# Kernel optimization log

Measured on AMD Instinct MI355X. Metric: run time of the kernel, lower is better.

The kernel has to match this reference:

```python
import jax, jax.numpy as jnp
import numpy as np
from jax import lax

DIM = 384
NH = 8
HD = DIM // NH
M = 16          # num_anchors
B = 16
HH = 64
WW = 64
N = HH * WW
STD = 0.02


def setup_inputs() -> dict:
    key = jax.random.key(0)
    ks = jax.random.split(key, 12)
    rn = lambda k, shape: (jax.random.normal(k, shape, jnp.float32) * STD)
    return {
        "x": jax.random.normal(ks[0], (B, N, DIM), jnp.float32),
        "H": HH,
        "W": WW,
        "saliency_w": rn(ks[1], (DIM, 1)),
        "saliency_b": jnp.zeros((1,), jnp.float32),
        "anchor_seeds": rn(ks[2], (1, M, DIM)),
        "w_q_agg": rn(ks[3], (DIM, DIM)),
        "w_kv_agg": rn(ks[4], (DIM, 2 * DIM)),
        "w_q_self": rn(ks[5], (DIM, DIM)),
        "w_kv_self": rn(ks[6], (DIM, 2 * DIM)),
        "w_q_bcast": rn(ks[7], (DIM, DIM)),
        "w_kv_bcast": rn(ks[8], (DIM, 2 * DIM)),
        "dw_kernel": rn(ks[9], (DIM, 1, 3, 3)),  # depthwise conv, OIHW with I=1
        "w_proj": rn(ks[10], (DIM, DIM)),
    }


def _mhsa(q_in, kv_in, wq, wkv):
    """Multi-head cross attention. q_in: [B,Lq,C], kv_in: [B,Lk,C]."""
    b, lq, c = q_in.shape
    lk = kv_in.shape[1]
    scale = HD ** -0.5
    q = (q_in @ wq).reshape(b, lq, NH, HD)
    kv = (kv_in @ wkv).reshape(b, lk, 2, NH, HD)
    k, v = kv[:, :, 0], kv[:, :, 1]
    attn = jnp.einsum("bqhd,bkhd->bhqk", q, k) * scale
    attn = jax.nn.softmax(attn, axis=-1)
    out = jnp.einsum("bhqk,bkhd->bqhd", attn, v).reshape(b, lq, c)
    return out


def reference(x, H, W, saliency_w, saliency_b, anchor_seeds,
              w_q_agg, w_kv_agg, w_q_self, w_kv_self,
              w_q_bcast, w_kv_bcast, dw_kernel, w_proj):
    b, n, c = x.shape
    # saliency gating
    sal = jax.nn.sigmoid(x @ saliency_w + saliency_b)  # [B,N,1]
    x_sal = x * sal
    # stage 1: anchors aggregate from saliency-gated tokens
    anchors = jnp.broadcast_to(anchor_seeds, (b, M, c))
    anchors = anchors + _mhsa(anchors, x_sal, w_q_agg, w_kv_agg)
    # stage 2: anchor self-attention
    anchors = anchors + _mhsa(anchors, anchors, w_q_self, w_kv_self)
    # stage 3: broadcast anchors back to all tokens
    global_out = _mhsa(x, anchors, w_q_bcast, w_kv_bcast)
    # depthwise 3x3 conv on the 2D token map
    x2d = x.reshape(b, H, W, c).transpose(0, 3, 1, 2)  # NCHW
    local = lax.conv_general_dilated(
        x2d, dw_kernel, window_strides=(1, 1), padding="SAME",
        feature_group_count=c,
        dimension_numbers=("NCHW", "OIHW", "NCHW"))
    local = local.transpose(0, 2, 3, 1).reshape(b, n, c)
    return (global_out + local) @ w_proj
```

## Files before the change

kernel.cpp:

```cpp
#include <hip/hip_runtime.h>
#include <hip/hip_bf16.h>

#define SCALE 0.14433756729740643f

typedef __attribute__((ext_vector_type(8))) short bf16x8;
typedef __attribute__((ext_vector_type(4))) float f32x4;

template <typename T> __device__ inline T cvt_from_f(float v);
template <> __device__ inline float cvt_from_f<float>(float v) { return v; }
template <> __device__ inline __hip_bfloat16 cvt_from_f<__hip_bfloat16>(float v) { return __float2bfloat16(v); }

__device__ inline void gload16(const void* g, void* l) {
  __builtin_amdgcn_global_load_lds((const __attribute__((address_space(1))) void*)g,
                                   (__attribute__((address_space(3))) void*)l, 16, 0, 0);
}

__device__ inline int xcd_flat(int nwg) {
  int flat = (blockIdx.z * gridDim.y + blockIdx.y) * gridDim.x + blockIdx.x;
  int per = nwg >> 3;
  return (flat & 7) * per + (flat >> 3);
}

__global__ __launch_bounds__(256) void prep(const float* __restrict__ x,
                                            const float* __restrict__ wsal,
                                            const float* __restrict__ bsal,
                                            __hip_bfloat16* __restrict__ xb,
                                            float* __restrict__ sal) {
  int wave = threadIdx.x >> 6, lane = threadIdx.x & 63;
  size_t row = (size_t)blockIdx.x * 4 + wave;
  const float* xr = x + row * 384;
  float xs[6];
  float part = 0.f;
#pragma unroll
  for (int j = 0; j < 6; j++) {
    int c = lane + 64 * j;
    xs[j] = xr[c];
    part += xs[j] * wsal[c];
  }
#pragma unroll
  for (int off = 32; off >= 1; off >>= 1) part += __shfl_xor(part, off);
  float s = 1.f / (1.f + __expf(-(part + bsal[0])));
#pragma unroll
  for (int j = 0; j < 6; j++) {
    int c = lane + 64 * j;
    xb[row * 384 + c] = __float2bfloat16(xs[j]);
  }
  if (lane == 0) sal[row] = s;
}

__global__ void wcast_tv(const float* __restrict__ w, __hip_bfloat16* __restrict__ wt) {
  int idx = blockIdx.x * 256 + threadIdx.x;
  if (idx >= 384 * 384) return;
  int n = idx / 384, k = idx % 384;
  wt[idx] = __float2bfloat16(w[(size_t)k * 768 + 384 + n]);
}

template <int K, typename OT, int BSHIFT>
__global__ __launch_bounds__(256) void gemm_mfma(const __hip_bfloat16* __restrict__ A,
                                                 const __hip_bfloat16* __restrict__ BT,
                                                 OT* __restrict__ out, int Ncols,
                                                 size_t btBatchStride) {
  __shared__ __align__(16) __hip_bfloat16 Asl[128][32];
  __shared__ __align__(16) __hip_bfloat16 Bsl[128][32];
  int nf = xcd_flat(gridDim.x * gridDim.y);
  int bX = nf % gridDim.x, bY = nf / gridDim.x;
  int tid = threadIdx.x;
  int lane = tid & 63;
  int w = tid >> 6;
  int wr = w >> 1, wc = w & 1;
  int fr = lane & 15, fq = lane >> 4;
  int rowBase = bY * 128, colBase = bX * 128;
  const __hip_bfloat16* BTb = BT + (size_t)(rowBase >> BSHIFT) * btBatchStride;

  int r1 = tid >> 2, kc1 = tid & 3;
  int r2 = (tid + 256) >> 2;

  char* aB1 = (char*)Asl + (size_t)(w * 64) * 16;
  char* aB2 = (char*)Asl + (size_t)(256 + w * 64) * 16;
  char* bB1 = (char*)Bsl + (size_t)(w * 64) * 16;
  char* bB2 = (char*)Bsl + (size_t)(256 + w * 64) * 16;

  const __hip_bfloat16* a1 = A + (size_t)(rowBase + r1) * K + kc1 * 8;
  const __hip_bfloat16* a2 = A + (size_t)(rowBase + r2) * K + kc1 * 8;
  const __hip_bfloat16* b1 = BTb + (size_t)(colBase + r1) * K + kc1 * 8;
  const __hip_bfloat16* b2 = BTb + (size_t)(colBase + r2) * K + kc1 * 8;

  f32x4 acc[4][4] = {};

  for (int kk = 0; kk < K; kk += 32) {
    gload16(a1 + kk, aB1);
    gload16(a2 + kk, aB2);
    gload16(b1 + kk, bB1);
    gload16(b2 + kk, bB2);
    __syncthreads();
    bf16x8 af[4], bfv[4];
#pragma unroll
    for (int m = 0; m < 4; m++) af[m] = *(const bf16x8*)&Asl[wr * 64 + m * 16 + fr][fq * 8];
#pragma unroll
    for (int n = 0; n < 4; n++) bfv[n] = *(const bf16x8*)&Bsl[wc * 64 + n * 16 + fr][fq * 8];
#pragma unroll
    for (int m = 0; m < 4; m++)
#pragma unroll
      for (int n = 0; n < 4; n++)
        acc[m][n] = __builtin_amdgcn_mfma_f32_16x16x32_bf16(af[m], bfv[n], acc[m][n], 0, 0, 0);
    __syncthreads();
  }

#pragma unroll
  for (int m = 0; m < 4; m++) {
    int row0 = rowBase + wr * 64 + m * 16 + fq * 4;
#pragma unroll
    for (int n = 0; n < 4; n++) {
      int col = colBase + wc * 64 + n * 16 + fr;
      f32x4 v = acc[m][n];
#pragma unroll
      for (int r = 0; r < 4; r++) out[(size_t)(row0 + r) * Ncols + col] = cvt_from_f<OT>(v[r]);
    }
  }
}

__global__ __launch_bounds__(256) void gemm_vlog(const __hip_bfloat16* __restrict__ A,
                                                 const __hip_bfloat16* __restrict__ BT,
                                                 __hip_bfloat16* __restrict__ vT,
                                                 __hip_bfloat16* __restrict__ lgT,
                                                 const float* __restrict__ rowScale) {
  constexpr int K = 384;
  __shared__ __align__(16) __hip_bfloat16 Asl[128][32];
  __shared__ __align__(16) __hip_bfloat16 Bsl[128][32];
  int nf = xcd_flat(2048);
  int bX = nf & 3, bY = nf >> 2;
  int tid = threadIdx.x;
  int lane = tid & 63;
  int w = tid >> 6;
  int wr = w >> 1, wc = w & 1;
  int fr = lane & 15, fq = lane >> 4;
  int rowBase = bY * 128, colBase = bX * 128;

  int r1 = tid >> 2, kc1 = tid & 3;
  int r2 = (tid + 256) >> 2;

  char* aB1 = (char*)Asl + (size_t)(w * 64) * 16;
  char* aB2 = (char*)Asl + (size_t)(256 + w * 64) * 16;
  char* bB1 = (char*)Bsl + (size_t)(w * 64) * 16;
  char* bB2 = (char*)Bsl + (size_t)(256 + w * 64) * 16;

  const __hip_bfloat16* a1 = A + (size_t)(rowBase + r1) * K + kc1 * 8;
  const __hip_bfloat16* a2 = A + (size_t)(rowBase + r2) * K + kc1 * 8;
  const __hip_bfloat16* b1 = BT + (size_t)(colBase + r1) * K + kc1 * 8;
  const __hip_bfloat16* b2 = BT + (size_t)(colBase + r2) * K + kc1 * 8;

  f32x4 acc[4][4] = {};

  for (int kk = 0; kk < K; kk += 32) {
    gload16(a1 + kk, aB1);
    gload16(a2 + kk, aB2);
    gload16(b1 + kk, bB1);
    gload16(b2 + kk, bB2);
    __syncthreads();
    bf16x8 af[4], bfv[4];
#pragma unroll
    for (int m = 0; m < 4; m++) af[m] = *(const bf16x8*)&Asl[wr * 64 + m * 16 + fr][fq * 8];
#pragma unroll
    for (int n = 0; n < 4; n++) bfv[n] = *(const bf16x8*)&Bsl[wc * 64 + n * 16 + fr][fq * 8];
#pragma unroll
    for (int m = 0; m < 4; m++)
#pragma unroll
      for (int n = 0; n < 4; n++)
        acc[m][n] = __builtin_amdgcn_mfma_f32_16x16x32_bf16(af[m], bfv[n], acc[m][n], 0, 0, 0);
    __syncthreads();
  }

  float sv[4][4];
#pragma unroll
  for (int m = 0; m < 4; m++)
#pragma unroll
    for (int r = 0; r < 4; r++)
      sv[m][r] = rowScale[rowBase + wr * 64 + m * 16 + fq * 4 + r];

  if (bX < 3) {
#pragma unroll
    for (int m = 0; m < 4; m++) {
      int row0 = rowBase + wr * 64 + m * 16 + fq * 4;
      int bb = row0 >> 12;
      int n0 = row0 & 4095;
#pragma unroll
      for (int n = 0; n < 4; n++) {
        int col = colBase + wc * 64 + n * 16 + fr;
        __hip_bfloat16 tb[4];
#pragma unroll
        for (int r = 0; r < 4; r++) tb[r] = __float2bfloat16(acc[m][n][r] * sv[m][r]);
        *(unsigned long long*)(vT + ((size_t)bb * 384 + col) * 4096 + n0) = *(unsigned long long*)tb;
      }
    }
  } else {
#pragma unroll
    for (int m = 0; m < 4; m++) {
      int row0 = rowBase + wr * 64 + m * 16 + fq * 4;
      int bb = row0 >> 12;
      int n0 = row0 & 4095;
#pragma unroll
      for (int n = 0; n < 4; n++) {
        int col = wc * 64 + n * 16 + fr;
        __hip_bfloat16 tb[4];
#pragma unroll
        for (int r = 0; r < 4; r++) tb[r] = __float2bfloat16(acc[m][n][r] * sv[m][r]);
        *(unsigned long long*)(lgT + ((size_t)bb * 128 + col) * 4096 + n0) = *(unsigned long long*)tb;
      }
    }
  }
}

__global__ __launch_bounds__(256) void gemm_pv(const __hip_bfloat16* __restrict__ PT,
                                               const __hip_bfloat16* __restrict__ vT,
                                               float* __restrict__ pbuf) {
  __shared__ __align__(16) __hip_bfloat16 Asl[128][32];
  __shared__ __align__(16) __hip_bfloat16 Bsl[128][32];
  int nf = xcd_flat(384);
  int bX = nf % 3, bY = (nf / 3) & 15, kz = nf / 48;
  int tid = threadIdx.x;
  int lane = tid & 63;
  int w = tid >> 6;
  int wr = w >> 1, wc = w & 1;
  int fr = lane & 15, fq = lane >> 4;
  int rowBase = bY * 128, colBase = bX * 128;
  const __hip_bfloat16* BTb = vT + (size_t)bY * 384 * 4096;

  int r1 = tid >> 2, kc1 = tid & 3;
  int r2 = (tid + 256) >> 2;

  char* aB1 = (char*)Asl + (size_t)(w * 64) * 16;
  char* aB2 = (char*)Asl + (size_t)(256 + w * 64) * 16;
  char* bB1 = (char*)Bsl + (size_t)(w * 64) * 16;
  char* bB2 = (char*)Bsl + (size_t)(256 + w * 64) * 16;

  const __hip_bfloat16* a1 = PT + (size_t)(rowBase + r1) * 4096 + kz * 512 + kc1 * 8;
  const __hip_bfloat16* a2 = PT + (size_t)(rowBase + r2) * 4096 + kz * 512 + kc1 * 8;
  const __hip_bfloat16* b1 = BTb + (size_t)(colBase + r1) * 4096 + kz * 512 + kc1 * 8;
  const __hip_bfloat16* b2 = BTb + (size_t)(colBase + r2) * 4096 + kz * 512 + kc1 * 8;

  f32x4 acc[4][4] = {};

  for (int kk = 0; kk < 512; kk += 32) {
    gload16(a1 + kk, aB1);
    gload16(a2 + kk, aB2);
    gload16(b1 + kk, bB1);
    gload16(b2 + kk, bB2);
    __syncthreads();
    bf16x8 af[4], bfv[4];
#pragma unroll
    for (int m = 0; m < 4; m++) af[m] = *(const bf16x8*)&Asl[wr * 64 + m * 16 + fr][fq * 8];
#pragma unroll
    for (int n = 0; n < 4; n++) bfv[n] = *(const bf16x8*)&Bsl[wc * 64 + n * 16 + fr][fq * 8];
#pragma unroll
    for (int m = 0; m < 4; m++)
#pragma unroll
      for (int n = 0; n < 4; n++)
        acc[m][n] = __builtin_amdgcn_mfma_f32_16x16x32_bf16(af[m], bfv[n], acc[m][n], 0, 0, 0);
    __syncthreads();
  }

  float* outz = pbuf + (size_t)kz * 786432;
#pragma unroll
  for (int m = 0; m < 4; m++) {
    int row0 = rowBase + wr * 64 + m * 16 + fq * 4;
#pragma unroll
    for (int n = 0; n < 4; n++) {
      int col = colBase + wc * 64 + n * 16 + fr;
      f32x4 v = acc[m][n];
#pragma unroll
      for (int r = 0; r < 4; r++) outz[(size_t)(row0 + r) * 384 + col] = v[r];
    }
  }
}

__global__ void anch_fix2(const float* __restrict__ pbuf, const float* __restrict__ seeds,
                          float* __restrict__ anch1) {
  int idx = blockIdx.x * 256 + threadIdx.x;
  int b = idx / 6144;
  int rem = idx - b * 6144;
  int m = rem / 384, c = rem - m * 384;
  int g = b * 128 + (c / 48) * 16 + m;
  const float* p = pbuf + (size_t)g * 384 + c;
  float s = 0.f;
#pragma unroll
  for (int z = 0; z < 8; z++) s += p[(size_t)z * 786432];
  anch1[idx] = seeds[rem] + s;
}

__global__ __launch_bounds__(256) void softmax_rows(const __hip_bfloat16* __restrict__ lgT,
                                                    __hip_bfloat16* __restrict__ PT) {
  int g = blockIdx.x;
  const __hip_bfloat16* row = lgT + (size_t)g * 4096;
  int tid = threadIdx.x, wv = tid >> 6, lane = tid & 63;
  __shared__ float redm[4], reds[4];
  float v[16];
  union { ulonglong2 u; __hip_bfloat16 h[8]; } L0, L1;
  L0.u = *(const ulonglong2*)(row + tid * 16);
  L1.u = *(const ulonglong2*)(row + tid * 16 + 8);
#pragma unroll
  for (int i = 0; i < 8; i++) {
    v[i] = __bfloat162float(L0.h[i]);
    v[8 + i] = __bfloat162float(L1.h[i]);
  }
  float mx = v[0];
#pragma unroll
  for (int i = 1; i < 16; i++) mx = fmaxf(mx, v[i]);
#pragma unroll
  for (int off = 1; off < 64; off <<= 1) mx = fmaxf(mx, __shfl_xor(mx, off));
  if (lane == 0) redm[wv] = mx;
  __syncthreads();
  mx = fmaxf(fmaxf(redm[0], redm[1]), fmaxf(redm[2], redm[3]));
  float s = 0.f;
#pragma unroll
  for (int i = 0; i < 16; i++) {
    v[i] = __expf(v[i] - mx);
    s += v[i];
  }
#pragma unroll
  for (int off = 1; off < 64; off <<= 1) s += __shfl_xor(s, off);
  if (lane == 0) reds[wv] = s;
  __syncthreads();
  s = (reds[0] + reds[1]) + (reds[2] + reds[3]);
  float inv = 1.f / s;
  __hip_bfloat16 tb[16];
#pragma unroll
  for (int i = 0; i < 16; i++) tb[i] = __float2bfloat16(v[i] * inv);
  __hip_bfloat16* op = PT + (size_t)g * 4096 + tid * 16;
  *(ulonglong2*)op = *(ulonglong2*)tb;
  *(ulonglong2*)(op + 8) = *(ulonglong2*)(tb + 8);
}

__global__ void fill_wl(const float* __restrict__ wkv, const float* __restrict__ qseed,
                        __hip_bfloat16* __restrict__ wvlT) {
  int idx = blockIdx.x * 256 + threadIdx.x;
  int hm = idx / 384, ci = idx - hm * 384;
  int h = hm >> 4, m = hm & 15;
  const float* wp = wkv + (size_t)ci * 768 + h * 48;
  const float* qp = qseed + m * 384 + h * 48;
  float acc = 0.f;
#pragma unroll
  for (int d = 0; d < 48; d++) acc += wp[d] * qp[d];
  wvlT[384 * 384 + idx] = __float2bfloat16(acc);
}

__global__ __launch_bounds__(256) void pgemm_conv(const __hip_bfloat16* __restrict__ A,
                                                  const __hip_bfloat16* __restrict__ wpbT,
                                                  const float* __restrict__ dwk,
                                                  __hip_bfloat16* __restrict__ A2) {
  constexpr int K = 384;
  __shared__ __align__(16) __hip_bfloat16 Asl[128][32];
  __shared__ __align__(16) __hip_bfloat16 Bsl[128][32];
  int tid = threadIdx.x;
  int lane = tid & 63;
  int w = tid >> 6;
  int wr = w >> 1, wc = w & 1;
  int fr = lane & 15, fq = lane >> 4;
  int rowBase = blockIdx.y * 128;
  const __hip_bfloat16* BTb = wpbT + (size_t)(rowBase >> 12) * (128 * 384);

  int r1 = tid >> 2, kc1 = tid & 3;
  int r2 = (tid + 256) >> 2;

  char* aB1 = (char*)Asl + (size_t)(w * 64) * 16;
  char* aB2 = (char*)Asl + (size_t)(256 + w * 64) * 16;
  char* bB1 = (char*)Bsl + (size_t)(w * 64) * 16;
  char* bB2 = (char*)Bsl + (size_t)(256 + w * 64) * 16;

  const __hip_bfloat16* a1 = A + (size_t)(rowBase + r1) * K + kc1 * 8;
  const __hip_bfloat16* a2 = A + (size_t)(rowBase + r2) * K + kc1 * 8;
  const __hip_bfloat16* b1 = BTb + (size_t)r1 * K + kc1 * 8;
  const __hip_bfloat16* b2 = BTb + (size_t)r2 * K + kc1 * 8;

  f32x4 acc[4][4] = {};

  for (int kk = 0; kk < K; kk += 32) {
    gload16(a1 + kk, aB1);
    gload16(a2 + kk, aB2);
    gload16(b1 + kk, bB1);
    gload16(b2 + kk, bB2);
    __syncthreads();
    bf16x8 af[4], bfv[4];
#pragma unroll
    for (int m = 0; m < 4; m++) af[m] = *(const bf16x8*)&Asl[wr * 64 + m * 16 + fr][fq * 8];
#pragma unroll
    for (int n = 0; n < 4; n++) bfv[n] = *(const bf16x8*)&Bsl[wc * 64 + n * 16 + fr][fq * 8];
#pragma unroll
    for (int m = 0; m < 4; m++)
#pragma unroll
      for (int n = 0; n < 4; n++)
        acc[m][n] = __builtin_amdgcn_mfma_f32_16x16x32_bf16(af[m], bfv[n], acc[m][n], 0, 0, 0);
    __syncthreads();
  }

#pragma unroll
  for (int m = 0; m < 4; m++) {
    int row0 = rowBase + wr * 64 + m * 16 + fq * 4;
#pragma unroll
    for (int n = 0; n < 4; n++) {
      int col = wc * 64 + n * 16 + fr;
      f32x4 v = acc[m][n];
      f32x4 mx = v;
#pragma unroll
      for (int off = 1; off < 16; off <<= 1)
#pragma unroll
        for (int r = 0; r < 4; r++) mx[r] = fmaxf(mx[r], __shfl_xor(mx[r], off));
      f32x4 e;
#pragma unroll
      for (int r = 0; r < 4; r++) e[r] = __expf(v[r] - mx[r]);
      f32x4 s = e;
#pragma unroll
      for (int off = 1; off < 16; off <<= 1)
#pragma unroll
        for (int r = 0; r < 4; r++) s[r] += __shfl_xor(s[r], off);
#pragma unroll
      for (int r = 0; r < 4; r++)
        A2[(size_t)(row0 + r) * 512 + 384 + col] = __float2bfloat16(e[r] / s[r]);
    }
  }

  int c0 = lane * 6;
  float kw[6][9];
#pragma unroll
  for (int i = 0; i < 6; i++)
#pragma unroll
    for (int ki = 0; ki < 9; ki++) kw[i][ki] = dwk[(c0 + i) * 9 + ki];
  int bb2 = rowBase >> 12;
  int p0 = rowBase & 4095;
  for (int it = 0; it < 32; it++) {
    int p = p0 + w * 32 + it;
    int y = p >> 6, wx = p & 63;
    size_t prow = (size_t)rowBase + w * 32 + it;
    float acc2[6] = {};
#pragma unroll
    for (int dy = -1; dy <= 1; dy++) {
      int yy = y + dy;
      if (yy < 0 || yy >= 64) continue;
#pragma unroll
      for (int dx = -1; dx <= 1; dx++) {
        int ww2 = wx + dx;
        if (ww2 < 0 || ww2 >= 64) continue;
        int ki = (dy + 1) * 3 + (dx + 1);
        const __hip_bfloat16* xp = A + ((size_t)(bb2 * 4096 + yy * 64 + ww2)) * 384 + c0;
#pragma unroll
        for (int i = 0; i < 6; i++) acc2[i] += __bfloat162float(xp[i]) * kw[i][ki];
      }
    }
    __hip_bfloat16 tb[6];
#pragma unroll
    for (int i = 0; i < 6; i++) tb[i] = __float2bfloat16(acc2[i]);
    __hip_bfloat16* gp = A2 + prow * 512 + c0;
    *(unsigned int*)(gp) = *(unsigned int*)(tb);
    *(unsigned int*)(gp + 2) = *(unsigned int*)(tb + 2);
    *(unsigned int*)(gp + 4) = *(unsigned int*)(tb + 4);
  }
}

__global__ __launch_bounds__(256) void anchor_proj2(const float* __restrict__ A,
                                                    const float* __restrict__ W,
                                                    float* __restrict__ out, int wstride,
                                                    int scaleCols) {
  int cs = blockIdx.x * 16;
  int b = blockIdx.y;
  __shared__ float a1[16][385];
  int tid = threadIdx.x;
  for (int idx = tid; idx < 6144; idx += 256) a1[idx / 384][idx % 384] = A[b * 6144 + idx];
  __syncthreads();
  int m = tid >> 4, cc = tid & 15;
  int col = cs + cc;
  const float* wp = W + col;
  float acc0 = 0.f, acc1 = 0.f, acc2 = 0.f, acc3 = 0.f;
#pragma unroll 4
  for (int k = 0; k < 384; k += 4) {
    acc0 += a1[m][k] * wp[(size_t)k * wstride];
    acc1 += a1[m][k + 1] * wp[(size_t)(k + 1) * wstride];
    acc2 += a1[m][k + 2] * wp[(size_t)(k + 2) * wstride];
    acc3 += a1[m][k + 3] * wp[(size_t)(k + 3) * wstride];
  }
  float acc = (acc0 + acc1) + (acc2 + acc3);
  if (col < scaleCols) acc *= SCALE;
  out[((size_t)b * 16 + m) * wstride + col] = acc;
}

__global__ __launch_bounds__(256) void anchor_proj_qkv(const float* __restrict__ A,
                                                       const float* __restrict__ Wq,
                                                       const float* __restrict__ Wkv,
                                                       float* __restrict__ q_out,
                                                       float* __restrict__ kv_out) {
  bool isQ = blockIdx.x < 24;
  int bx = isQ ? blockIdx.x : blockIdx.x - 24;
  const float* W = isQ ? Wq : Wkv;
  float* outp = isQ ? q_out : kv_out;
  int wstride = isQ ? 384 : 768;
  float scale = isQ ? SCALE : 1.f;
  int cs = bx * 16;
  int b = blockIdx.y;
  __shared__ float a1[16][385];
  int tid = threadIdx.x;
  for (int idx = tid; idx < 6144; idx += 256) a1[idx / 384][idx % 384] = A[b * 6144 + idx];
  __syncthreads();
  int m = tid >> 4, cc = tid & 15;
  int col = cs + cc;
  const float* wp = W + col;
  float acc0 = 0.f, acc1 = 0.f, acc2 = 0.f, acc3 = 0.f;
#pragma unroll 4
  for (int k = 0; k < 384; k += 4) {
    acc0 += a1[m][k] * wp[(size_t)k * wstride];
    acc1 += a1[m][k + 1] * wp[(size_t)(k + 1) * wstride];
    acc2 += a1[m][k + 2] * wp[(size_t)(k + 2) * wstride];
    acc3 += a1[m][k + 3] * wp[(size_t)(k + 3) * wstride];
  }
  float acc = ((acc0 + acc1) + (acc2 + acc3)) * scale;
  outp[((size_t)b * 16 + m) * wstride + col] = acc;
}

__global__ void self_attn(const float* __restrict__ qsf, const float* __restrict__ kvs,
                          const float* __restrict__ anch1, float* __restrict__ anch2) {
  int h = blockIdx.x & 7, b = blockIdx.x >> 3;
  __shared__ float qs[16][48], ks[16][48], vs[16][48], p[16][17];
  int tid = threadIdx.x;
  for (int idx = tid; idx < 768; idx += 256) {
    int m = idx / 48, d = idx % 48;
    qs[m][d] = qsf[(b * 16 + m) * 384 + h * 48 + d];
    ks[m][d] = kvs[(b * 16 + m) * 768 + h * 48 + d];
    vs[m][d] = kvs[(b * 16 + m) * 768 + 384 + h * 48 + d];
  }
  __syncthreads();
  {
    int mq = tid >> 4, mk = tid & 15;
    float acc = 0.f;
    for (int d = 0; d < 48; d++) acc += qs[mq][d] * ks[mk][d];
    p[mq][mk] = acc;
  }
  __syncthreads();
  if (tid < 16) {
    float mx = -1e30f;
    for (int mk = 0; mk < 16; mk++) mx = fmaxf(mx, p[tid][mk]);
    float sum = 0.f;
    for (int mk = 0; mk < 16; mk++) {
      float e = __expf(p[tid][mk] - mx);
      p[tid][mk] = e;
      sum += e;
    }
    float inv = 1.f / sum;
    for (int mk = 0; mk < 16; mk++) p[tid][mk] *= inv;
  }
  __syncthreads();
  for (int idx = tid; idx < 768; idx += 256) {
    int m = idx / 48, d = idx % 48;
    float acc = 0.f;
    for (int mk = 0; mk < 16; mk++) acc += p[m][mk] * vs[mk][d];
    int c = h * 48 + d;
    anch2[(b * 16 + m) * 384 + c] = anch1[(b * 16 + m) * 384 + c] + acc;
  }
}

__global__ void fill_wb(const float* __restrict__ wq, const float* __restrict__ wproj,
                        const float* __restrict__ kvb,
                        __hip_bfloat16* __restrict__ wpbT,
                        __hip_bfloat16* __restrict__ bt2) {
  int idx = blockIdx.x * 256 + threadIdx.x;
  if (idx < 786432) {
    int b = idx / 49152;
    int rem = idx - b * 49152;
    int hm = rem / 384, k = rem - hm * 384;
    int h = hm >> 4, m = hm & 15;
    const float* kp = kvb + ((size_t)(b * 16 + m)) * 768 + h * 48;
    const float* wp = wq + (size_t)k * 384 + h * 48;
    float acc = 0.f;
#pragma unroll
    for (int d = 0; d < 48; d++) acc += wp[d] * kp[d];
    wpbT[idx] = __float2bfloat16(acc);
  } else {
    int j = idx - 786432;
    int b = j / 196608;
    int rem = j - b * 196608;
    int cp = rem / 512, k2 = rem - cp * 512;
    float v;
    if (k2 < 384) {
      v = wproj[(size_t)k2 * 384 + cp];
    } else {
      int hm = k2 - 384, h = hm >> 4, m = hm & 15;
      const float* vp = kvb + ((size_t)(b * 16 + m)) * 768 + 384 + h * 48;
      const float* wp2 = wproj + (size_t)(h * 48) * 384 + cp;
      v = 0.f;
#pragma unroll
      for (int d = 0; d < 48; d++) v += vp[d] * wp2[(size_t)d * 384];
    }
    bt2[j] = __float2bfloat16(v);
  }
}

extern "C" void kernel_launch(void* const* d_in, const int* in_sizes, int n_in,
                              void* d_out, int out_size, void* d_ws, size_t ws_size,
                              hipStream_t stream) {
  (void)in_sizes; (void)n_in; (void)out_size; (void)ws_size;
  const float* x = (const float*)d_in[0];
  const float* wsal = (const float*)d_in[3];
  const float* bsal = (const float*)d_in[4];
  const float* seeds = (const float*)d_in[5];
  const float* w_q_agg = (const float*)d_in[6];
  const float* w_kv_agg = (const float*)d_in[7];
  const float* w_q_self = (const float*)d_in[8];
  const float* w_kv_self = (const float*)d_in[9];
  const float* w_q_bcast = (const float*)d_in[10];
  const float* w_kv_bcast = (const float*)d_in[11];
  const float* dwk = (const float*)d_in[12];
  const float* w_proj = (const float*)d_in[13];
  float* out = (float*)d_out;

  char* ws = (char*)d_ws;
  size_t off = 0;
  auto take = [&](size_t bytes) -> void* {
    void* p = ws + off;
    off += (bytes + 255) & ~(size_t)255;
    return p;
  };
  __hip_bfloat16* xb = (__hip_bfloat16*)take(50331648);
  __hip_bfloat16* vT = (__hip_bfloat16*)take(50331648);
  char* lgRegion = (char*)take(33554432);
  __hip_bfloat16* PT = (__hip_bfloat16*)take(16777216);
  float* qseed = (float*)take(24576);
  float* sal = (float*)take(262144);
  float* anch1 = (float*)take(393216);
  float* anch2 = (float*)take(393216);
  float* q_self = (float*)take(393216);
  float* kv_self = (float*)take(786432);
  float* kv_b = (float*)take(786432);
  __hip_bfloat16* wvlT = (__hip_bfloat16*)take(393216);
  __hip_bfloat16* wpbT = (__hip_bfloat16*)take(1572864);
  __hip_bfloat16* bt2 = (__hip_bfloat16*)take(6291456);
  __hip_bfloat16* logitsT = (__hip_bfloat16*)lgRegion;
  float* pbuf = (float*)lgRegion;
  __hip_bfloat16* A2 = vT;

  prep<<<16384, 256, 0, stream>>>(x, wsal, bsal, xb, sal);
  anchor_proj2<<<dim3(24, 1), 256, 0, stream>>>(seeds, w_q_agg, qseed, 384, 384);
  wcast_tv<<<576, 256, 0, stream>>>(w_kv_agg, wvlT);
  fill_wl<<<192, 256, 0, stream>>>(w_kv_agg, qseed, wvlT);
  gemm_vlog<<<dim3(4, 512), 256, 0, stream>>>(xb, wvlT, vT, logitsT, sal);
  softmax_rows<<<2048, 256, 0, stream>>>(logitsT, PT);
  gemm_pv<<<dim3(3, 16, 8), 256, 0, stream>>>(PT, vT, pbuf);
  anch_fix2<<<384, 256, 0, stream>>>(pbuf, seeds, anch1);
  anchor_proj_qkv<<<dim3(72, 16), 256, 0, stream>>>(anch1, w_q_self, w_kv_self, q_self, kv_self);
  self_attn<<<128, 256, 0, stream>>>(q_self, kv_self, anch1, anch2);
  anchor_proj2<<<dim3(48, 16), 256, 0, stream>>>(anch2, w_kv_bcast, kv_b, 768, 384);
  fill_wb<<<15360, 256, 0, stream>>>(w_q_bcast, w_proj, kv_b, wpbT, bt2);
  pgemm_conv<<<dim3(1, 512), 256, 0, stream>>>(xb, wpbT, dwk, A2);
  gemm_mfma<512, float, 12><<<dim3(3, 512), 256, 0, stream>>>(A2, bt2, out, 384, (size_t)384 * 512);
}
```

Measured before the change: 373.0 us.

## Split fill_wb into transpose and per-head fused weight kernels with shared reuse

Replaces the single element-per-thread fill_wb kernel with three kernels: a tiled shared-memory transpose of w_proj into bt2 (launched early, independent of anchors), and per-(head,batch) kernels that stage the anchor K/V slices in shared memory and compute 16 anchor outputs per thread with vectorized weight loads. This is meant to remove redundant global reads and uncoalesced strided accesses in the weight-folding step. The per-head kernels launch only 128 blocks, so they may underuse the GPU.

```diff
diff --git a/kernel.cpp b/kernel.cpp
--- a/kernel.cpp
+++ b/kernel.cpp
@@ -341,6 +341,96 @@
 #pragma unroll
   for (int d = 0; d < 48; d++) acc += wp[d] * qp[d];
   wvlT[384 * 384 + idx] = __float2bfloat16(acc);
+}
+
+__global__ __launch_bounds__(256) void wtrans(const float* __restrict__ wproj,
+                                              __hip_bfloat16* __restrict__ bt2) {
+  __shared__ float t[64][65];
+  int kt = blockIdx.x * 64, ct = blockIdx.y * 64;
+  int tid = threadIdx.x;
+  int c = tid & 63, r4 = tid >> 6;
+#pragma unroll
+  for (int i = 0; i < 16; i++) {
+    int r = i * 4 + r4;
+    t[r][c] = wproj[(size_t)(kt + r) * 384 + ct + c];
+  }
+  __syncthreads();
+  __hip_bfloat16 vals[16];
+#pragma unroll
+  for (int i = 0; i < 16; i++) vals[i] = __float2bfloat16(t[c][i * 4 + r4]);
+  for (int b = blockIdx.z * 4; b < blockIdx.z * 4 + 4; b++) {
+    __hip_bfloat16* dst = bt2 + (size_t)b * 196608;
+#pragma unroll
+    for (int i = 0; i < 16; i++) {
+      int rr = i * 4 + r4;
+      dst[(size_t)(ct + rr) * 512 + kt + c] = vals[i];
+    }
+  }
+}
+
+__global__ __launch_bounds__(256) void fill_wv2(const float* __restrict__ wproj,
+                                                const float* __restrict__ kvb,
+                                                __hip_bfloat16* __restrict__ bt2) {
+  int h = blockIdx.x, b = blockIdx.y;
+  __shared__ float vbs[16][48];
+  int tid = threadIdx.x;
+  for (int idx = tid; idx < 768; idx += 256) {
+    int m = idx / 48, d = idx % 48;
+    vbs[m][d] = kvb[(size_t)(b * 16 + m) * 768 + 384 + h * 48 + d];
+  }
+  __syncthreads();
+  for (int cp = tid; cp < 384; cp += 256) {
+    float acc[16] = {};
+    for (int d = 0; d < 48; d++) {
+      float wv = wproj[(size_t)(h * 48 + d) * 384 + cp];
+#pragma unroll
+      for (int m = 0; m < 16; m++) acc[m] += vbs[m][d] * wv;
+    }
+    __hip_bfloat16 tb[16];
+#pragma unroll
+    for (int m = 0; m < 16; m++) tb[m] = __float2bfloat16(acc[m]);
+    __hip_bfloat16* dst = bt2 + (size_t)b * 196608 + (size_t)cp * 512 + 384 + h * 16;
+    *(ulonglong2*)dst = *(ulonglong2*)tb;
+    *(ulonglong2*)(dst + 8) = *(ulonglong2*)(tb + 8);
+  }
+}
+
+__global__ __launch_bounds__(256) void fill_wpb2(const float* __restrict__ wq,
+                                                 const float* __restrict__ kvb,
+                                                 __hip_bfloat16* __restrict__ wpbT) {
+  int h = blockIdx.x, b = blockIdx.y;
+  __shared__ float kbs[16][48];
+  __shared__ __hip_bfloat16 obuf[16][264];
+  int tid = threadIdx.x;
+  for (int idx = tid; idx < 768; idx += 256) {
+    int m = idx / 48, d = idx % 48;
+    kbs[m][d] = kvb[(size_t)(b * 16 + m) * 768 + h * 48 + d];
+  }
+  __syncthreads();
+  for (int kbase = 0; kbase < 384; kbase += 256) {
+    int chunk = (kbase == 0) ? 256 : 128;
+    if (tid < chunk) {
+      int k = kbase + tid;
+      const float4* wp = (const float4*)(wq + (size_t)k * 384 + h * 48);
+      float acc[16] = {};
+#pragma unroll
+      for (int dq = 0; dq < 12; dq++) {
+        float4 wv = wp[dq];
+#pragma unroll
+        for (int m = 0; m < 16; m++)
+          acc[m] += kbs[m][dq * 4] * wv.x + kbs[m][dq * 4 + 1] * wv.y +
+                    kbs[m][dq * 4 + 2] * wv.z + kbs[m][dq * 4 + 3] * wv.w;
+      }
+#pragma unroll
+      for (int m = 0; m < 16; m++) obuf[m][tid] = __float2bfloat16(acc[m]);
+    }
+    __syncthreads();
+    for (int widx = tid; widx < 16 * chunk; widx += 256) {
+      int m = widx / chunk, kk = widx - m * chunk;
+      wpbT[(size_t)b * 49152 + (size_t)(h * 16 + m) * 384 + kbase + kk] = obuf[m][kk];
+    }
+    __syncthreads();
+  }
 }
 
 __global__ __launch_bounds__(256) void pgemm_conv(const __hip_bfloat16* __restrict__ A,
@@ -551,42 +641,6 @@
     for (int mk = 0; mk < 16; mk++) acc += p[m][mk] * vs[mk][d];
     int c = h * 48 + d;
     anch2[(b * 16 + m) * 384 + c] = anch1[(b * 16 + m) * 384 + c] + acc;
-  }
-}
-
-__global__ void fill_wb(const float* __restrict__ wq, const float* __restrict__ wproj,
-                        const float* __restrict__ kvb,
-                        __hip_bfloat16* __restrict__ wpbT,
-                        __hip_bfloat16* __restrict__ bt2) {
-  int idx = blockIdx.x * 256 + threadIdx.x;
-  if (idx < 786432) {
-    int b = idx / 49152;
-    int rem = idx - b * 49152;
-    int hm = rem / 384, k = rem - hm * 384;
-    int h = hm >> 4, m = hm & 15;
-    const float* kp = kvb + ((size_t)(b * 16 + m)) * 768 + h * 48;
-    const float* wp = wq + (size_t)k * 384 + h * 48;
-    float acc = 0.f;
-#pragma unroll
-    for (int d = 0; d < 48; d++) acc += wp[d] * kp[d];
-    wpbT[idx] = __float2bfloat16(acc);
-  } else {
-    int j = idx - 786432;
-    int b = j / 196608;
-    int rem = j - b * 196608;
-    int cp = rem / 512, k2 = rem - cp * 512;
-    float v;
-    if (k2 < 384) {
-      v = wproj[(size_t)k2 * 384 + cp];
-    } else {
-      int hm = k2 - 384, h = hm >> 4, m = hm & 15;
-      const float* vp = kvb + ((size_t)(b * 16 + m)) * 768 + 384 + h * 48;
-      const float* wp2 = wproj + (size_t)(h * 48) * 384 + cp;
-      v = 0.f;
-#pragma unroll
-      for (int d = 0; d < 48; d++) v += vp[d] * wp2[(size_t)d * 384];
-    }
-    bt2[j] = __float2bfloat16(v);
   }
 }
 
@@ -637,6 +691,7 @@
   anchor_proj2<<<dim3(24, 1), 256, 0, stream>>>(seeds, w_q_agg, qseed, 384, 384);
   wcast_tv<<<576, 256, 0, stream>>>(w_kv_agg, wvlT);
   fill_wl<<<192, 256, 0, stream>>>(w_kv_agg, qseed, wvlT);
+  wtrans<<<dim3(6, 6, 4), 256, 0, stream>>>(w_proj, bt2);
   gemm_vlog<<<dim3(4, 512), 256, 0, stream>>>(xb, wvlT, vT, logitsT, sal);
   softmax_rows<<<2048, 256, 0, stream>>>(logitsT, PT);
   gemm_pv<<<dim3(3, 16, 8), 256, 0, stream>>>(PT, vT, pbuf);
@@ -644,7 +699,8 @@
   anchor_proj_qkv<<<dim3(72, 16), 256, 0, stream>>>(anch1, w_q_self, w_kv_self, q_self, kv_self);
   self_attn<<<128, 256, 0, stream>>>(q_self, kv_self, anch1, anch2);
   anchor_proj2<<<dim3(48, 16), 256, 0, stream>>>(anch2, w_kv_bcast, kv_b, 768, 384);
-  fill_wb<<<15360, 256, 0, stream>>>(w_q_bcast, w_proj, kv_b, wpbT, bt2);
+  fill_wpb2<<<dim3(8, 16), 256, 0, stream>>>(w_q_bcast, kv_b, wpbT);
+  fill_wv2<<<dim3(8, 16), 256, 0, stream>>>(w_proj, kv_b, bt2);
   pgemm_conv<<<dim3(1, 512), 256, 0, stream>>>(xb, wpbT, dwk, A2);
   gemm_mfma<512, float, 12><<<dim3(3, 512), 256, 0, stream>>>(A2, bt2, out, 384, (size_t)384 * 512);
 }
```

After: 352.9 us. -5.4%, faster.
